# Optimization experiments

Hardware: AMD Instinct MI355X
Metric: run time of the kernel (lower is better)

Reference implementation:

```python
import jax, jax.numpy as jnp
import numpy as np

N, N_FEAT, F1, F2, F3, N_Z = 4096, 512, 256, 128, 64, 16
SLOPE = 0.2
NEG = -9e16


def _xavier(key, shape):
    std = (2.0 / (shape[0] + shape[1])) ** 0.5
    return jax.random.normal(key, shape, dtype=jnp.float32) * std


def setup_inputs() -> dict:
    key = jax.random.key(0)
    ks = jax.random.split(key, 20)
    x = jax.random.normal(ks[0], (N, N_FEAT), dtype=jnp.float32)
    adj = jax.random.randint(ks[1], (N, N), 0, 2, dtype=jnp.int32)
    dims = [N_FEAT, F1, F2, F3, N_Z, F3, F2, F1, N_FEAT]
    inp = {"x": x, "adj": adj}
    for i in range(8):
        fi, fo = dims[i], dims[i + 1]
        inp[f"w{i+1}"] = _xavier(ks[2 + 2 * i], (fi, fo))
        inp[f"a{i+1}"] = _xavier(ks[3 + 2 * i], (2 * fo, 1))
    return inp


def _gat(x, adj_pos, w, a):
    h = x @ w                               # [N, f_out]
    f = h.shape[1]
    src = h @ a[:f]                         # [N, 1]
    tgt = h @ a[f:]                         # [N, 1]
    e = jax.nn.leaky_relu(src + tgt.T, SLOPE)  # [N, N] broadcast score sum
    e = jnp.where(adj_pos, e, NEG)
    attn = jax.nn.softmax(e, axis=-1)
    return attn @ h                          # [N, f_out]


def reference(x, adj, w1, a1, w2, a2, w3, a3, w4, a4, w5, a5, w6, a6, w7, a7, w8, a8):
    adj_pos = adj > 0
    h1 = _gat(x, adj_pos, w1, a1)
    h2 = _gat(h1, adj_pos, w2, a2)
    h3 = _gat(h2, adj_pos, w3, a3)
    h4 = _gat(h3, adj_pos, w4, a4)
    h5 = _gat(h4, adj_pos, w5, a5)
    h6 = _gat(h5, adj_pos, w6, a6)
    h7 = _gat(h6, adj_pos, w7, a7)
    x_bar = _gat(h7, adj_pos, w8, a8)
    return (x_bar, h1, h2, h3, h4)
```

## Files before the change

### kernel.cpp

```cpp
#include <hip/hip_runtime.h>
#include <hip/hip_bf16.h>
#include <hip/hip_fp16.h>


#define NROWS 4096
#define TMC 12.0f

typedef __attribute__((ext_vector_type(8))) short v8s;
typedef __attribute__((ext_vector_type(8))) _Float16 v8h;
typedef __attribute__((ext_vector_type(2))) _Float16 h2v;
typedef __attribute__((ext_vector_type(4))) float v4f;

__device__ inline unsigned short f2bf(float x) {
  union { float f; unsigned u; } v; v.f = x;
  unsigned r = v.u + 0x7fffu + ((v.u >> 16) & 1u);
  return (unsigned short)(r >> 16);
}

__global__ void pack_adj(const int* __restrict__ adj, unsigned long long* __restrict__ bits) {
  int row = blockIdx.x;
  int lane = threadIdx.x & 63, wave = threadIdx.x >> 6;
  for (int w = wave; w < 64; w += 4) {
    unsigned long long m = __ballot(adj[(size_t)row * NROWS + w * 64 + lane] > 0);
    if (lane == 0) bits[row * 64 + w] = m;
  }
}

struct WTArgs { const float* src[8]; unsigned short* dst[8]; int K[8]; int F[8]; };
__global__ void transpose_w(WTArgs A) {
  int z = blockIdx.z;
  const float* in = A.src[z];
  unsigned short* out = A.dst[z];
  int R = A.K[z], C = A.F[z];
  __shared__ unsigned short tile[32][33];
  int c0 = blockIdx.x * 32, r0 = blockIdx.y * 32;
  if (c0 >= C || r0 >= R) return;
#pragma unroll
  for (int dy = 0; dy < 32; dy += 8) {
    int r = r0 + threadIdx.y + dy, c = c0 + threadIdx.x;
    if (r < R && c < C) tile[threadIdx.y + dy][threadIdx.x] = f2bf(in[(size_t)r * C + c]);
  }
  __syncthreads();
#pragma unroll
  for (int dy = 0; dy < 32; dy += 8) {
    int c = c0 + threadIdx.y + dy, r = r0 + threadIdx.x;
    if (r < R && c < C) out[(size_t)c * R + r] = tile[threadIdx.x][threadIdx.y + dy];
  }
}

__global__ __launch_bounds__(128) void gemm_xw(const float* __restrict__ A,
                                               const unsigned short* __restrict__ BT,
                                               float* __restrict__ C,
                                               unsigned short* __restrict__ HTt,
                                               int K, int Nf) {
  __shared__ unsigned short zone[64 * 36];
  int lane = threadIdx.x & 63, wave = threadIdx.x >> 6;
  int quad = lane >> 4, l16 = lane & 15;
  int row0 = blockIdx.x * 32 + wave * 16;
  int col0 = blockIdx.y * 64;
  int nf = Nf - col0; nf = nf > 64 ? 4 : (nf + 15) / 16;
  v4f acc[4] = {{0.f,0.f,0.f,0.f},{0.f,0.f,0.f,0.f},{0.f,0.f,0.f,0.f},{0.f,0.f,0.f,0.f}};
  for (int k0 = 0; k0 < K; k0 += 32) {
    int kk = k0 + quad * 8;
    v8s a = {0,0,0,0,0,0,0,0};
    if (kk < K) {
      float4 f0 = *(const float4*)(A + (size_t)(row0 + l16) * K + kk);
      float4 f1 = *(const float4*)(A + (size_t)(row0 + l16) * K + kk + 4);
      union { v8s s; __hip_bfloat162 h[4]; } ua;
      ua.h[0] = __float22bfloat162_rn(make_float2(f0.x, f0.y));
      ua.h[1] = __float22bfloat162_rn(make_float2(f0.z, f0.w));
      ua.h[2] = __float22bfloat162_rn(make_float2(f1.x, f1.y));
      ua.h[3] = __float22bfloat162_rn(make_float2(f1.z, f1.w));
      a = ua.s;
    }
    for (int t = 0; t < nf; t++) {
      v8s b = {0,0,0,0,0,0,0,0};
      if (kk < K) b = *(const v8s*)(BT + (size_t)(col0 + t * 16 + l16) * K + kk);
      acc[t] = __builtin_amdgcn_mfma_f32_16x16x32_bf16(a, b, acc[t], 0, 0, 0);
    }
  }
  for (int t = 0; t < nf; t++) {
#pragma unroll
    for (int r = 0; r < 4; r++) {
      float v = acc[t][r];
      C[(size_t)(row0 + quad * 4 + r) * Nf + col0 + t * 16 + l16] = v;
      union { _Float16 h; unsigned short s; } cv; cv.h = (_Float16)v;
      zone[(t * 16 + l16) * 36 + wave * 16 + quad * 4 + r] = cv.s;
    }
  }
  __syncthreads();
  unsigned* dst = (unsigned*)(HTt + (size_t)(blockIdx.x) * Nf * 32 + (size_t)col0 * 32);
  const unsigned* zsrc = (const unsigned*)zone;
  int total = nf * 256;
  for (int idx = threadIdx.x; idx < total; idx += 128) {
    int f = idx >> 4, jp = idx & 15;
    dst[idx] = zsrc[f * 18 + jp];
  }
}

__global__ void gemv_srctgt(const float* __restrict__ H, const float* __restrict__ a,
                            float* __restrict__ src, unsigned short* __restrict__ Ev16,
                            unsigned short* __restrict__ Gv16, int f) {
  int row = blockIdx.x * 4 + (threadIdx.x >> 6);
  int lane = threadIdx.x & 63;
  float s = 0.f, t = 0.f;
  for (int k = lane; k < f; k += 64) {
    float h = H[(size_t)row * f + k];
    s += h * a[k];
    t += h * a[f + k];
  }
#pragma unroll
  for (int off = 32; off; off >>= 1) { s += __shfl_down(s, off); t += __shfl_down(t, off); }
  if (lane == 0) {
    src[row] = s;
    union { _Float16 h; unsigned short u; } ce, cg;
    ce.h = (_Float16)(__expf(t - TMC) * 16384.f);
    cg.h = (_Float16)(__expf(0.2f * (t - TMC)) * 16.f);
    Ev16[row] = ce.u;
    Gv16[row] = cg.u;
  }
}

template<int NF>
__global__ __launch_bounds__(256) void pass2f(const unsigned* __restrict__ adjW,
                                              const float* __restrict__ src,
                                              const unsigned short* __restrict__ Ev16,
                                              const unsigned short* __restrict__ Gv16,
                                              const unsigned short* __restrict__ HTt,
                                              float* __restrict__ out,
                                              float* __restrict__ part,
                                              float* __restrict__ ls0,
                                              float* __restrict__ part_ls, int F, int js) {
  const int W = NF * 16, Wp = W + 4;
  __shared__ float zone[32 * Wp];
  int lane = threadIdx.x & 63, wave = threadIdx.x >> 6;
  int quad = lane >> 4, l16 = lane & 15;
  int i0 = blockIdx.x * 32;
  int fc0 = blockIdx.y * W;
  const size_t F32 = (size_t)F * 32;
  int jrange = NROWS / js;
  int jlen = jrange / 4;
  int jstart = blockIdx.z * jrange + wave * jlen;

  h2v Ai2[2], Bi2[2];
  const unsigned* arow[2];
#pragma unroll
  for (int ni = 0; ni < 2; ni++) {
    int i = i0 + ni * 16 + l16;
    float sp = src[i] + TMC;
    float m = sp > 0.f ? sp : 0.2f * sp;
    _Float16 ai = (_Float16)(__expf(sp - m) * 0x1p-14f);
    _Float16 bi = (_Float16)(__expf(0.2f * sp - m) * 0x1p-4f);
    Ai2[ni] = (h2v){ai, ai};
    Bi2[ni] = (h2v){bi, bi};
    arow[ni] = adjW + (size_t)i * 128;
  }
  const v8h ones = {(_Float16)1.f, (_Float16)1.f, (_Float16)1.f, (_Float16)1.f,
                    (_Float16)1.f, (_Float16)1.f, (_Float16)1.f, (_Float16)1.f};
  v4f acc[2][NF], accl[2];
#pragma unroll
  for (int ni = 0; ni < 2; ni++) {
    accl[ni] = (v4f){0.f, 0.f, 0.f, 0.f};
#pragma unroll
    for (int t = 0; t < NF; t++) acc[ni][t] = (v4f){0.f, 0.f, 0.f, 0.f};
  }

  for (int j0 = jstart; j0 < jstart + jlen; j0 += 128) {
    uint4 aw[2];
    aw[0] = *(const uint4*)(arow[0] + (j0 >> 5));
    aw[1] = *(const uint4*)(arow[1] + (j0 >> 5));
    unsigned awa[2][4] = {{aw[0].x, aw[0].y, aw[0].z, aw[0].w},
                          {aw[1].x, aw[1].y, aw[1].z, aw[1].w}};
#pragma unroll
    for (int u = 0; u < 4; u++) {
      int ju = j0 + u * 32;
      int jb = ju + quad * 8;
      union { v8s s; h2v h2[4]; } ue, ug;
      ue.s = *(const v8s*)(Ev16 + jb);
      ug.s = *(const v8s*)(Gv16 + jb);
      const unsigned short* bp =
          HTt + (size_t)(ju >> 5) * F32 + (size_t)(fc0 + l16) * 32 + quad * 8;
      union { v8s s; v8h h; } bfr[NF];
#pragma unroll
      for (int t = 0; t < NF; t++) bfr[t].s = *(const v8s*)(bp + t * 512);
#pragma unroll
      for (int ni = 0; ni < 2; ni++) {
        unsigned bb = awa[ni][u] >> (quad * 8);
        union { v8h h; unsigned u32[4]; } ua;
#pragma unroll
        for (int p = 0; p < 4; p++) {
          h2v w2 = __builtin_elementwise_max(Ai2[ni] * ue.h2[p], Bi2[ni] * ug.h2[p]);
          unsigned msk = (((bb >> (2 * p)) & 1u) ? 0x0000FFFFu : 0u)
                       | (((bb >> (2 * p + 1)) & 1u) ? 0xFFFF0000u : 0u);
          union { h2v h2; unsigned u; } tw; tw.h2 = w2;
          ua.u32[p] = tw.u & msk;
        }
#pragma unroll
        for (int t = 0; t < NF; t++)
          acc[ni][t] = __builtin_amdgcn_mfma_f32_16x16x32_f16(ua.h, bfr[t].h, acc[ni][t], 0, 0, 0);
        accl[ni] = __builtin_amdgcn_mfma_f32_16x16x32_f16(ua.h, ones, accl[ni], 0, 0, 0);
      }
    }
  }

  for (int w = 0; w < 4; w++) {
    if (wave == w) {
#pragma unroll
      for (int ni = 0; ni < 2; ni++) {
#pragma unroll
        for (int t = 0; t < NF; t++)
#pragma unroll
          for (int r = 0; r < 4; r++) {
            int idx = (ni * 16 + quad * 4 + r) * Wp + t * 16 + l16;
            if (w == 0) zone[idx] = acc[ni][t][r];
            else        zone[idx] += acc[ni][t][r];
          }
        if (l16 == 0) {
#pragma unroll
          for (int r = 0; r < 4; r++) {
            int idx = (ni * 16 + quad * 4 + r) * Wp + W;
            if (w == 0) zone[idx] = accl[ni][r];
            else        zone[idx] += accl[ni][r];
          }
        }
      }
    }
    __syncthreads();
  }

  if (js == 1) {
    if (threadIdx.x < 32) zone[threadIdx.x * Wp + W] = 1.0f / zone[threadIdx.x * Wp + W];
    __syncthreads();
    for (int idx = threadIdx.x; idx < 32 * W; idx += 256) {
      int rrow = idx / W, ccol = idx - rrow * W;
      out[(size_t)(i0 + rrow) * F + fc0 + ccol] = zone[rrow * Wp + ccol] * zone[rrow * Wp + W];
    }
  } else {
    float* dst = (blockIdx.z == 0) ? out : part + (size_t)(blockIdx.z - 1) * NROWS * F;
    for (int idx = threadIdx.x; idx < 32 * W; idx += 256) {
      int rrow = idx / W, ccol = idx - rrow * W;
      dst[(size_t)(i0 + rrow) * F + fc0 + ccol] = zone[rrow * Wp + ccol];
    }
    if (threadIdx.x < 32) {
      float l = zone[threadIdx.x * Wp + W];
      if (blockIdx.z == 0) ls0[i0 + threadIdx.x] = l;
      else part_ls[(size_t)(blockIdx.z - 1) * NROWS + i0 + threadIdx.x] = l;
    }
  }
}

__global__ void reduce_add(const float* __restrict__ part, const float* __restrict__ part_ls,
                           const float* __restrict__ ls0, float* __restrict__ out, int n, int F,
                           int nslab) {
  int i = blockIdx.x * 256 + threadIdx.x;
  if (i < n) {
    int row = i / F;
    float s = out[i];
    float l = ls0[row];
    for (int z = 0; z < nslab; z++) s += part[(size_t)z * n + i];
    for (int z = 0; z < nslab; z++) l += part_ls[(size_t)z * NROWS + row];
    out[i] = s / l;
  }
}

static void launch_pass2(int NF, dim3 grid, const unsigned* adjW, const float* src,
                         const unsigned short* Ev16, const unsigned short* Gv16,
                         const unsigned short* HTt, float* out, float* part, float* ls0,
                         float* part_ls, int F, int js, hipStream_t stream) {
  switch (NF) {
    case 8: pass2f<8><<<grid, 256, 0, stream>>>(adjW, src, Ev16, Gv16, HTt, out, part, ls0,
                                                part_ls, F, js); break;
    case 4: pass2f<4><<<grid, 256, 0, stream>>>(adjW, src, Ev16, Gv16, HTt, out, part, ls0,
                                                part_ls, F, js); break;
    default: pass2f<1><<<grid, 256, 0, stream>>>(adjW, src, Ev16, Gv16, HTt, out, part, ls0,
                                                 part_ls, F, js); break;
  }
}

extern "C" void kernel_launch(void* const* d_in, const int* in_sizes, int n_in,
                              void* d_out, int out_size, void* d_ws, size_t ws_size,
                              hipStream_t stream) {
  static const int fin[8]  = {512, 256, 128, 64, 16, 64, 128, 256};
  static const int fout[8] = {256, 128, 64, 16, 64, 128, 256, 512};

  const float* x = (const float*)d_in[0];
  const int* adj = (const int*)d_in[1];
  char* ws = (char*)d_ws;
  unsigned long long* bits = (unsigned long long*)(ws);
  unsigned short* WTall = (unsigned short*)(ws + (2u << 20));
  float* H            = (float*)(ws + (6u << 20));
  unsigned short* HTt = (unsigned short*)(ws + (14u << 20));
  float* srcv    = (float*)(ws + (19u << 20));
  float* ls0     = (float*)(ws + (19u << 20) + (16u << 10));
  float* part_ls = (float*)(ws + (19u << 20) + (32u << 10));
  unsigned short* Ev16 = (unsigned short*)(ws + (19u << 20) + (160u << 10));
  unsigned short* Gv16 = (unsigned short*)(ws + (19u << 20) + (168u << 10));
  float* o5    = (float*)(ws + (20u << 20));
  float* o6    = (float*)(ws + (21u << 20));
  float* o7    = (float*)(ws + (23u << 20));
  float* part = H;

  float* outp = (float*)d_out;
  float* xbar = outp;
  float* h1 = outp + (size_t)NROWS * 512;
  float* h2 = h1 + (size_t)NROWS * 256;
  float* h3 = h2 + (size_t)NROWS * 128;
  float* h4 = h3 + (size_t)NROWS * 64;

  float* louts[8] = {h1, h2, h3, h4, o5, o6, o7, xbar};
  const float* lins[8] = {x, h1, h2, h3, h4, o5, o6, o7};

  unsigned short* WT[8];
  { size_t off = 0;
    for (int t = 0; t < 8; t++) { WT[t] = WTall + off; off += (size_t)fin[t] * fout[t]; } }

  pack_adj<<<dim3(4096), dim3(256), 0, stream>>>(adj, bits);

  WTArgs wa;
  for (int t = 0; t < 8; t++) {
    wa.src[t] = (const float*)d_in[2 + 2 * t];
    wa.dst[t] = WT[t];
    wa.K[t] = fin[t];
    wa.F[t] = fout[t];
  }
  transpose_w<<<dim3(16, 16, 8), dim3(32, 8), 0, stream>>>(wa);

  for (int t = 0; t < 8; t++) {
    int K = fin[t], F = fout[t];
    const float* At = (const float*)d_in[3 + 2 * t];
    const float* Xin = lins[t];
    float* Ot = louts[t];

    int NF, js;
    if (F == 512)      { NF = 4; js = 1; }
    else if (F == 256) { NF = 8; js = 2; }
    else if (F == 128) { NF = 8; js = 4; }
    else if (F == 64)  { NF = 4; js = 4; }
    else               { NF = 1; js = 4; }
    int fc = F / (16 * NF);
    dim3 grid(128, fc, js);

    gemm_xw<<<dim3(128, (F + 63) / 64), dim3(128), 0, stream>>>(Xin, WT[t], H, HTt, K, F);
    gemv_srctgt<<<dim3(1024), dim3(256), 0, stream>>>(H, At, srcv, Ev16, Gv16, F);
    launch_pass2(NF, grid, (const unsigned*)bits, srcv, Ev16, Gv16, HTt, Ot, part,
                 ls0, part_ls, F, js, stream);
    if (js > 1)
      reduce_add<<<dim3((NROWS * F + 255) / 256), dim3(256), 0, stream>>>(part, part_ls, ls0, Ot,
                                                                          NROWS * F, F, js - 1);
  }
}
```

Before: 477.3 us.

## Double-buffer operand loads in attention pass and widen F=512 tile

The pass-2 inner loop now steps through 32-column chunks and double-buffers them with A/B register sets. The next chunk's HTt fragments, E/G values and adjacency words are loaded while MFMAs run on the current chunk, which is meant to hide global-load latency. The adjacency mask is now built with shift-and-arithmetic-shift sign extension instead of conditionals. For F=512 the per-block feature count goes from 4 to 8 tiles, which halves the grid in that dimension and raises register pressure.

After: 511.2 us. 7.1% more time.

```diff
diff --git a/kernel.cpp b/kernel.cpp
--- a/kernel.cpp
+++ b/kernel.cpp
@@ -165,42 +165,67 @@
     for (int t = 0; t < NF; t++) acc[ni][t] = (v4f){0.f, 0.f, 0.f, 0.f};
   }
 
-  for (int j0 = jstart; j0 < jstart + jlen; j0 += 128) {
-    uint4 aw[2];
-    aw[0] = *(const uint4*)(arow[0] + (j0 >> 5));
-    aw[1] = *(const uint4*)(arow[1] + (j0 >> 5));
-    unsigned awa[2][4] = {{aw[0].x, aw[0].y, aw[0].z, aw[0].w},
-                          {aw[1].x, aw[1].y, aw[1].z, aw[1].w}};
-#pragma unroll
-    for (int u = 0; u < 4; u++) {
-      int ju = j0 + u * 32;
-      int jb = ju + quad * 8;
-      union { v8s s; h2v h2[4]; } ue, ug;
-      ue.s = *(const v8s*)(Ev16 + jb);
-      ug.s = *(const v8s*)(Gv16 + jb);
-      const unsigned short* bp =
-          HTt + (size_t)(ju >> 5) * F32 + (size_t)(fc0 + l16) * 32 + quad * 8;
-      union { v8s s; v8h h; } bfr[NF];
-#pragma unroll
-      for (int t = 0; t < NF; t++) bfr[t].s = *(const v8s*)(bp + t * 512);
-#pragma unroll
-      for (int ni = 0; ni < 2; ni++) {
-        unsigned bb = awa[ni][u] >> (quad * 8);
-        union { v8h h; unsigned u32[4]; } ua;
-#pragma unroll
-        for (int p = 0; p < 4; p++) {
-          h2v w2 = __builtin_elementwise_max(Ai2[ni] * ue.h2[p], Bi2[ni] * ug.h2[p]);
-          unsigned msk = (((bb >> (2 * p)) & 1u) ? 0x0000FFFFu : 0u)
-                       | (((bb >> (2 * p + 1)) & 1u) ? 0xFFFF0000u : 0u);
-          union { h2v h2; unsigned u; } tw; tw.h2 = w2;
-          ua.u32[p] = tw.u & msk;
-        }
-#pragma unroll
-        for (int t = 0; t < NF; t++)
-          acc[ni][t] = __builtin_amdgcn_mfma_f32_16x16x32_f16(ua.h, bfr[t].h, acc[ni][t], 0, 0, 0);
-        accl[ni] = __builtin_amdgcn_mfma_f32_16x16x32_f16(ua.h, ones, accl[ni], 0, 0, 0);
+  union bun { v8s s; v8h h; };
+  const unsigned short* bpw =
+      HTt + ((size_t)(jstart >> 5)) * F32 + (size_t)(fc0 + l16) * 32 + quad * 8;
+  const unsigned short* evp = Ev16 + jstart + quad * 8;
+  const unsigned short* gvp = Gv16 + jstart + quad * 8;
+  int awi = jstart >> 5;
+  int nIt = jlen >> 5;
+
+  bun bfA[NF], bfB[NF];
+  v8s ueA, ugA, ueB, ugB;
+  unsigned awA[2], awB[2];
+
+#pragma unroll
+  for (int t = 0; t < NF; t++) bfA[t].s = *(const v8s*)(bpw + t * 512);
+  ueA = *(const v8s*)evp; ugA = *(const v8s*)gvp;
+  awA[0] = arow[0][awi]; awA[1] = arow[1][awi];
+
+  auto compute = [&](const bun (&bf)[NF], v8s ues, v8s ugs, const unsigned (&aww)[2]) {
+    union { v8s s; h2v h2[4]; } ue, ug;
+    ue.s = ues; ug.s = ugs;
+#pragma unroll
+    for (int ni = 0; ni < 2; ni++) {
+      unsigned bb = aww[ni] >> (quad * 8);
+      union { v8h h; unsigned u32[4]; } ua;
+#pragma unroll
+      for (int p = 0; p < 4; p++) {
+        h2v w2 = __builtin_elementwise_max(Ai2[ni] * ue.h2[p], Bi2[ni] * ug.h2[p]);
+        unsigned lo = (unsigned)((int)(bb << (31 - 2 * p)) >> 31);
+        unsigned hi = (unsigned)((int)(bb << (30 - 2 * p)) >> 31);
+        union { h2v h2; unsigned u; } tw; tw.h2 = w2;
+        ua.u32[p] = tw.u & ((lo & 0x0000FFFFu) | (hi & 0xFFFF0000u));
       }
-    }
+#pragma unroll
+      for (int t = 0; t < NF; t++)
+        acc[ni][t] = __builtin_amdgcn_mfma_f32_16x16x32_f16(ua.h, bf[t].h, acc[ni][t], 0, 0, 0);
+      accl[ni] = __builtin_amdgcn_mfma_f32_16x16x32_f16(ua.h, ones, accl[ni], 0, 0, 0);
+    }
+  };
+
+  for (int it = 0; it < nIt; it += 2) {
+    {
+      const unsigned short* bp1 = bpw + F32;
+#pragma unroll
+      for (int t = 0; t < NF; t++) bfB[t].s = *(const v8s*)(bp1 + t * 512);
+      ueB = *(const v8s*)(evp + 32); ugB = *(const v8s*)(gvp + 32);
+      awB[0] = arow[0][awi + 1]; awB[1] = arow[1][awi + 1];
+    }
+    compute(bfA, ueA, ugA, awA);
+    {
+      size_t adv = (it + 2 < nIt) ? 2 : 0;
+      const unsigned short* bp2 = bpw + adv * F32;
+      const unsigned short* ev2 = evp + adv * 32;
+      const unsigned short* gv2 = gvp + adv * 32;
+      int aw2 = awi + (int)adv;
+#pragma unroll
+      for (int t = 0; t < NF; t++) bfA[t].s = *(const v8s*)(bp2 + t * 512);
+      ueA = *(const v8s*)ev2; ugA = *(const v8s*)gv2;
+      awA[0] = arow[0][aw2]; awA[1] = arow[1][aw2];
+    }
+    compute(bfB, ueB, ugB, awB);
+    bpw += 2 * F32; evp += 64; gvp += 64; awi += 2;
   }
 
   for (int w = 0; w < 4; w++) {
@@ -332,7 +357,7 @@
     float* Ot = louts[t];
 
     int NF, js;
-    if (F == 512)      { NF = 4; js = 1; }
+    if (F == 512)      { NF = 8; js = 1; }
     else if (F == 256) { NF = 8; js = 2; }
     else if (F == 128) { NF = 8; js = 4; }
     else if (F == 64)  { NF = 4; js = 4; }
```
